# Performance work log

Hardware: AMD Instinct MI355X
Metric: run time of the kernel (lower is better)

## Reference

```python
import jax, jax.numpy as jnp
import numpy as np

NUM_EXPERTS = 16
NUM_K = 2


def setup_inputs() -> dict:
    key = jax.random.key(0)
    k1, k2 = jax.random.split(key)
    x = jax.random.normal(k1, (8, 8192, 1024), dtype=jnp.float32)
    W = jax.random.normal(k2, (NUM_EXPERTS, 1024), dtype=jnp.float32) * (1.0 / np.sqrt(1024))
    b = jnp.zeros((NUM_EXPERTS,), dtype=jnp.float32)
    return {"x": x, "W": W, "b": b}


def reference(x, W, b):
    # logits: [B, S, E]
    logits = jnp.einsum('bsd,ed->bse', x, W) + b
    weights = jax.nn.softmax(logits, axis=-1)
    # top-k over experts, then scatter values back into a sparse gate mask
    topk_vals, topk_idx = jax.lax.top_k(weights, NUM_K)  # [B, S, k]
    # one-hot scatter (E is small, so [B,S,k,E] intermediate is cheap)
    gated = (jax.nn.one_hot(topk_idx, NUM_EXPERTS, dtype=weights.dtype)
             * topk_vals[..., None]).sum(axis=-2)  # [B, S, E]
    # permute(2, 0, 1): [E, B, S]
    return gated.transpose(2, 0, 1), weights.transpose(2, 0, 1)
```

## Files before the change

### kernel.cpp

```cpp
#include <hip/hip_runtime.h>
#include <math.h>


typedef __attribute__((ext_vector_type(8))) short frag8;
typedef __attribute__((ext_vector_type(4))) float f32x4;
typedef unsigned short u16;
typedef unsigned int u32;

constexpr int D    = 1024;
constexpr int D4   = 256;
constexpr int NE   = 16;
constexpr int NTOK = 65536;
constexpr int TPB  = 256;
constexpr int TOKS = 64;
constexpr int NCH  = 16;
constexpr int RS   = 72;
constexpr int PL   = TOKS * RS;
constexpr int LSTR = 20;

__device__ __forceinline__ u16 bf_rne(float v, float* back) {
    u32 u = __float_as_uint(v);
    u32 r = (u + 0x7FFFu + ((u >> 16) & 1u)) >> 16;
    *back = __uint_as_float(r << 16);
    return (u16)r;
}

__device__ __forceinline__ void split3(float v, u16& a, u16& b, u16& c) {
    float t;
    a = bf_rne(v, &t); float r = v - t;
    b = bf_rne(r, &t); r -= t;
    c = bf_rne(r, &t);
}

__device__ __forceinline__ void loadX(const float4* __restrict__ xg4, int c,
                                      int tid, float4* pf) {
    const int col = tid & 15;
    #pragma unroll
    for (int s = 0; s < 4; ++s) {
        const int r = (s << 4) + (tid >> 4);
        pf[s] = xg4[r * D4 + c * 16 + col];
    }
}

__device__ __forceinline__ void loadB(const u16* __restrict__ wb, int c,
                                      frag8 Bf[2][3]) {
    #pragma unroll
    for (int ks = 0; ks < 2; ++ks)
        #pragma unroll
        for (int p = 0; p < 3; ++p)
            Bf[ks][p] = *(const frag8*)(wb + p * (NE * D) + (c * 2 + ks) * 32);
}

__device__ __forceinline__ void stage(const float4* pf, u16* __restrict__ lbuf,
                                      int tid) {
    const int col = tid & 15;
    #pragma unroll
    for (int s = 0; s < 4; ++s) {
        const int r = (s << 4) + (tid >> 4);
        u16 h[3][4];
        split3(pf[s].x, h[0][0], h[1][0], h[2][0]);
        split3(pf[s].y, h[0][1], h[1][1], h[2][1]);
        split3(pf[s].z, h[0][2], h[1][2], h[2][2]);
        split3(pf[s].w, h[0][3], h[1][3], h[2][3]);
        #pragma unroll
        for (int p = 0; p < 3; ++p) {
            u32 lo = (u32)h[p][0] | ((u32)h[p][1] << 16);
            u32 hi = (u32)h[p][2] | ((u32)h[p][3] << 16);
            *(uint2*)&lbuf[p * PL + r * RS + (col << 2)] = make_uint2(lo, hi);
        }
    }
}

__device__ __forceinline__ void compute(const u16* __restrict__ lbuf,
                                        const frag8 Bf[2][3],
                                        int l, int w, f32x4& acc) {
    const u16* arow = lbuf + (w * 16 + (l & 15)) * RS + (l >> 4) * 8;
    #pragma unroll
    for (int ks = 0; ks < 2; ++ks) {
        frag8 a1 = *(const frag8*)(arow + 0 * PL + ks * 32);
        frag8 a2 = *(const frag8*)(arow + 1 * PL + ks * 32);
        frag8 a3 = *(const frag8*)(arow + 2 * PL + ks * 32);
        acc = __builtin_amdgcn_mfma_f32_16x16x32_bf16(a3, Bf[ks][0], acc, 0, 0, 0);
        acc = __builtin_amdgcn_mfma_f32_16x16x32_bf16(a2, Bf[ks][1], acc, 0, 0, 0);
        acc = __builtin_amdgcn_mfma_f32_16x16x32_bf16(a1, Bf[ks][2], acc, 0, 0, 0);
        acc = __builtin_amdgcn_mfma_f32_16x16x32_bf16(a2, Bf[ks][0], acc, 0, 0, 0);
        acc = __builtin_amdgcn_mfma_f32_16x16x32_bf16(a1, Bf[ks][1], acc, 0, 0, 0);
        acc = __builtin_amdgcn_mfma_f32_16x16x32_bf16(a1, Bf[ks][0], acc, 0, 0, 0);
    }
}

__global__ void prep_w(const float* __restrict__ W, u16* __restrict__ wsp) {
    const int i = blockIdx.x * 256 + threadIdx.x;
    if (i < NE * D) {
        u16 a, b, c;
        split3(W[i], a, b, c);
        wsp[i] = a; wsp[NE * D + i] = b; wsp[2 * NE * D + i] = c;
    }
}

__global__ __launch_bounds__(TPB, 2) void gating_mfma(
    const float* __restrict__ x,
    const float* __restrict__ bias,
    const u16* __restrict__ wsp,
    float* __restrict__ out)
{
    __shared__ __align__(16) u16 xls[2 * 3 * PL];
    const int tid = threadIdx.x;
    const int l = tid & 63, w = tid >> 6;
    const long blockTok = (long)blockIdx.x * TOKS;
    const float4* __restrict__ xg4 = (const float4*)x + blockTok * D4;
    const u16* __restrict__ wb = wsp + (l & 15) * D + (l >> 4) * 8;

    float4 pfA[4], pfB[4];
    frag8 BfA[2][3], BfB[2][3];
    loadX(xg4, 0, tid, pfA);
    loadB(wb, 0, BfA);
    f32x4 acc = {0.f, 0.f, 0.f, 0.f};

    #pragma unroll 1
    for (int c = 0; c < NCH; c += 2) {
        stage(pfA, xls, tid);
        __syncthreads();
        loadX(xg4, c + 1, tid, pfB);
        loadB(wb, c + 1, BfB);
        compute(xls, BfA, l, w, acc);

        stage(pfB, xls + 3 * PL, tid);
        __syncthreads();
        if (c + 2 < NCH) { loadX(xg4, c + 2, tid, pfA); loadB(wb, c + 2, BfA); }
        compute(xls + 3 * PL, BfB, l, w, acc);
    }

    float* lb = (float*)xls;
    #pragma unroll
    for (int r = 0; r < 4; ++r)
        lb[(w * 16 + (l >> 4) * 4 + r) * LSTR + (l & 15)] = acc[r];
    __syncthreads();

    float logits[NE];
    float mx = -INFINITY;
    #pragma unroll
    for (int e = 0; e < NE; ++e) {
        logits[e] = lb[l * LSTR + e] + bias[e];
        mx = fmaxf(mx, logits[e]);
    }
    float wt[NE];
    float s = 0.0f;
    #pragma unroll
    for (int e = 0; e < NE; ++e) { wt[e] = __expf(logits[e] - mx); s += wt[e]; }
    const float inv = 1.0f / s;
    #pragma unroll
    for (int e = 0; e < NE; ++e) wt[e] *= inv;

    float b1 = -1.0f; int i1 = 0;
    float b2 = -1.0f; int i2 = 0;
    #pragma unroll
    for (int e = 0; e < NE; ++e) {
        if (wt[e] > b1)      { b2 = b1; i2 = i1; b1 = wt[e]; i1 = e; }
        else if (wt[e] > b2) { b2 = wt[e]; i2 = e; }
    }

    float* __restrict__ out0 = out;
    float* __restrict__ out1 = out + (long)NE * NTOK;
    #pragma unroll
    for (int i = 0; i < 4; ++i) {
        const int e = w * 4 + i;
        const float g = (e == i1) ? b1 : ((e == i2) ? b2 : 0.0f);
        out0[(long)e * NTOK + blockTok + l] = g;
        out1[(long)e * NTOK + blockTok + l] = wt[e];
    }
}

extern "C" void kernel_launch(void* const* d_in, const int* in_sizes, int n_in,
                              void* d_out, int out_size, void* d_ws, size_t ws_size,
                              hipStream_t stream) {
    const float* x = (const float*)d_in[0];
    const float* W = (const float*)d_in[1];
    const float* b = (const float*)d_in[2];
    float* out = (float*)d_out;
    u16* wsp = (u16*)d_ws;

    prep_w<<<64, 256, 0, stream>>>(W, wsp);
    gating_mfma<<<NTOK / TOKS, TPB, 0, stream>>>(x, b, wsp, out);
}
```

Baseline: 381.3 us.

## Stream raw fp32 x into swizzled LDS via async loads, split at MFMA time

Replaces the register-prefetch path, which split x into three bf16 planes before writing them to LDS, with direct global-to-LDS async loads of the raw fp32 tiles. The tiles are stored with an XOR column swizzle, and each lane splits its own fragment into bf16 parts just before the MFMAs. This cuts LDS footprint and VGPR pressure, so launch bounds rise to four blocks per CU, and it removes the register staging round trip. The cost is that the split arithmetic now sits on the compute side. Correctness also relies on the barrier waiting for the async LDS writes to finish.

```diff
diff --git a/kernel.cpp b/kernel.cpp
--- a/kernel.cpp
+++ b/kernel.cpp
@@ -8,14 +8,12 @@
 typedef unsigned int u32;
 
 constexpr int D    = 1024;
-constexpr int D4   = 256;
 constexpr int NE   = 16;
 constexpr int NTOK = 65536;
 constexpr int TPB  = 256;
 constexpr int TOKS = 64;
 constexpr int NCH  = 16;
-constexpr int RS   = 72;
-constexpr int PL   = TOKS * RS;
+constexpr int BUFF = 4096;
 constexpr int LSTR = 20;
 
 __device__ __forceinline__ u16 bf_rne(float v, float* back) {
@@ -32,14 +30,20 @@
     c = bf_rne(r, &t);
 }
 
-__device__ __forceinline__ void loadX(const float4* __restrict__ xg4, int c,
-                                      int tid, float4* pf) {
-    const int col = tid & 15;
-    #pragma unroll
-    for (int s = 0; s < 4; ++s) {
-        const int r = (s << 4) + (tid >> 4);
-        pf[s] = xg4[r * D4 + c * 16 + col];
-    }
+__device__ __forceinline__ void split2pk(float lo, float hi,
+                                         u32& p1, u32& p2, u32& p3) {
+    u16 a0, b0, c0, a1, b1, c1;
+    split3(lo, a0, b0, c0);
+    split3(hi, a1, b1, c1);
+    p1 = (u32)a0 | ((u32)a1 << 16);
+    p2 = (u32)b0 | ((u32)b1 << 16);
+    p3 = (u32)c0 | ((u32)c1 << 16);
+}
+
+__device__ __forceinline__ void async16(const float* g, float* l) {
+    __builtin_amdgcn_global_load_lds(
+        (const __attribute__((address_space(1))) void*)g,
+        (__attribute__((address_space(3))) void*)l, 16, 0, 0);
 }
 
 __device__ __forceinline__ void loadB(const u16* __restrict__ wb, int c,
@@ -51,41 +55,30 @@
             Bf[ks][p] = *(const frag8*)(wb + p * (NE * D) + (c * 2 + ks) * 32);
 }
 
-__device__ __forceinline__ void stage(const float4* pf, u16* __restrict__ lbuf,
-                                      int tid) {
-    const int col = tid & 15;
-    #pragma unroll
-    for (int s = 0; s < 4; ++s) {
-        const int r = (s << 4) + (tid >> 4);
-        u16 h[3][4];
-        split3(pf[s].x, h[0][0], h[1][0], h[2][0]);
-        split3(pf[s].y, h[0][1], h[1][1], h[2][1]);
-        split3(pf[s].z, h[0][2], h[1][2], h[2][2]);
-        split3(pf[s].w, h[0][3], h[1][3], h[2][3]);
-        #pragma unroll
-        for (int p = 0; p < 3; ++p) {
-            u32 lo = (u32)h[p][0] | ((u32)h[p][1] << 16);
-            u32 hi = (u32)h[p][2] | ((u32)h[p][3] << 16);
-            *(uint2*)&lbuf[p * PL + r * RS + (col << 2)] = make_uint2(lo, hi);
-        }
-    }
-}
-
-__device__ __forceinline__ void compute(const u16* __restrict__ lbuf,
-                                        const frag8 Bf[2][3],
-                                        int l, int w, f32x4& acc) {
-    const u16* arow = lbuf + (w * 16 + (l & 15)) * RS + (l >> 4) * 8;
+union Pk { u32 d[4]; frag8 f; };
+
+__device__ __forceinline__ void computeChunk(const float* __restrict__ buf,
+                                             const frag8 Bf[2][3],
+                                             int rtok, int xsw, int cbb,
+                                             f32x4& acc) {
+    const float* arow = buf + rtok * 64;
     #pragma unroll
     for (int ks = 0; ks < 2; ++ks) {
-        frag8 a1 = *(const frag8*)(arow + 0 * PL + ks * 32);
-        frag8 a2 = *(const frag8*)(arow + 1 * PL + ks * 32);
-        frag8 a3 = *(const frag8*)(arow + 2 * PL + ks * 32);
-        acc = __builtin_amdgcn_mfma_f32_16x16x32_bf16(a3, Bf[ks][0], acc, 0, 0, 0);
-        acc = __builtin_amdgcn_mfma_f32_16x16x32_bf16(a2, Bf[ks][1], acc, 0, 0, 0);
-        acc = __builtin_amdgcn_mfma_f32_16x16x32_bf16(a1, Bf[ks][2], acc, 0, 0, 0);
-        acc = __builtin_amdgcn_mfma_f32_16x16x32_bf16(a2, Bf[ks][0], acc, 0, 0, 0);
-        acc = __builtin_amdgcn_mfma_f32_16x16x32_bf16(a1, Bf[ks][1], acc, 0, 0, 0);
-        acc = __builtin_amdgcn_mfma_f32_16x16x32_bf16(a1, Bf[ks][0], acc, 0, 0, 0);
+        const int c0 = (cbb + ks * 8) ^ xsw;
+        const int c1 = (cbb + ks * 8 + 1) ^ xsw;
+        const float4 f0 = *(const float4*)(arow + c0 * 4);
+        const float4 f1 = *(const float4*)(arow + c1 * 4);
+        Pk P1, P2, P3;
+        split2pk(f0.x, f0.y, P1.d[0], P2.d[0], P3.d[0]);
+        split2pk(f0.z, f0.w, P1.d[1], P2.d[1], P3.d[1]);
+        split2pk(f1.x, f1.y, P1.d[2], P2.d[2], P3.d[2]);
+        split2pk(f1.z, f1.w, P1.d[3], P2.d[3], P3.d[3]);
+        acc = __builtin_amdgcn_mfma_f32_16x16x32_bf16(P3.f, Bf[ks][0], acc, 0, 0, 0);
+        acc = __builtin_amdgcn_mfma_f32_16x16x32_bf16(P2.f, Bf[ks][1], acc, 0, 0, 0);
+        acc = __builtin_amdgcn_mfma_f32_16x16x32_bf16(P1.f, Bf[ks][2], acc, 0, 0, 0);
+        acc = __builtin_amdgcn_mfma_f32_16x16x32_bf16(P2.f, Bf[ks][0], acc, 0, 0, 0);
+        acc = __builtin_amdgcn_mfma_f32_16x16x32_bf16(P1.f, Bf[ks][1], acc, 0, 0, 0);
+        acc = __builtin_amdgcn_mfma_f32_16x16x32_bf16(P1.f, Bf[ks][0], acc, 0, 0, 0);
     }
 }
 
@@ -98,43 +91,66 @@
     }
 }
 
-__global__ __launch_bounds__(TPB, 2) void gating_mfma(
+__global__ __launch_bounds__(TPB, 4) void gating_mfma(
     const float* __restrict__ x,
     const float* __restrict__ bias,
     const u16* __restrict__ wsp,
     float* __restrict__ out)
 {
-    __shared__ __align__(16) u16 xls[2 * 3 * PL];
+    __shared__ __align__(16) float xls[2 * BUFF];
     const int tid = threadIdx.x;
-    const int l = tid & 63, w = tid >> 6;
+    const int l   = tid & 63;
+    const int wvu = __builtin_amdgcn_readfirstlane(tid >> 6);
     const long blockTok = (long)blockIdx.x * TOKS;
-    const float4* __restrict__ xg4 = (const float4*)x + blockTok * D4;
+
+    const float* gp[4];
+    #pragma unroll
+    for (int i = 0; i < 4; ++i) {
+        const int s  = wvu * 256 + i * 64 + l;
+        const int r  = s >> 4;
+        const int cb = (s & 15) ^ (r & 15);
+        gp[i] = x + (blockTok + r) * D + cb * 4;
+    }
+
     const u16* __restrict__ wb = wsp + (l & 15) * D + (l >> 4) * 8;
-
-    float4 pfA[4], pfB[4];
+    const int rtok = wvu * 16 + (l & 15);
+    const int xsw  = l & 15;
+    const int cbb  = (l >> 4) * 2;
+
     frag8 BfA[2][3], BfB[2][3];
-    loadX(xg4, 0, tid, pfA);
+    #pragma unroll
+    for (int i = 0; i < 4; ++i)
+        async16((float*)gp[i], &xls[wvu * 1024 + i * 256]);
     loadB(wb, 0, BfA);
     f32x4 acc = {0.f, 0.f, 0.f, 0.f};
 
     #pragma unroll 1
     for (int c = 0; c < NCH; c += 2) {
-        stage(pfA, xls, tid);
         __syncthreads();
-        loadX(xg4, c + 1, tid, pfB);
-        loadB(wb, c + 1, BfB);
-        compute(xls, BfA, l, w, acc);
-
-        stage(pfB, xls + 3 * PL, tid);
+        if (true) {
+            #pragma unroll
+            for (int i = 0; i < 4; ++i)
+                async16((float*)(gp[i] + (c + 1) * 64),
+                        &xls[BUFF + wvu * 1024 + i * 256]);
+            loadB(wb, c + 1, BfB);
+        }
+        computeChunk(xls, BfA, rtok, xsw, cbb, acc);
+
         __syncthreads();
-        if (c + 2 < NCH) { loadX(xg4, c + 2, tid, pfA); loadB(wb, c + 2, BfA); }
-        compute(xls + 3 * PL, BfB, l, w, acc);
+        if (c + 2 < NCH) {
+            #pragma unroll
+            for (int i = 0; i < 4; ++i)
+                async16((float*)(gp[i] + (c + 2) * 64),
+                        &xls[wvu * 1024 + i * 256]);
+            loadB(wb, c + 2, BfA);
+        }
+        computeChunk(xls + BUFF, BfB, rtok, xsw, cbb, acc);
     }
 
     float* lb = (float*)xls;
     #pragma unroll
     for (int r = 0; r < 4; ++r)
-        lb[(w * 16 + (l >> 4) * 4 + r) * LSTR + (l & 15)] = acc[r];
+        lb[(wvu * 16 + (l >> 4) * 4 + r) * LSTR + (l & 15)] = acc[r];
     __syncthreads();
 
     float logits[NE];
@@ -164,7 +180,7 @@
     float* __restrict__ out1 = out + (long)NE * NTOK;
     #pragma unroll
     for (int i = 0; i < 4; ++i) {
-        const int e = w * 4 + i;
+        const int e = wvu * 4 + i;
         const float g = (e == i1) ? b1 : ((e == i2) ? b2 : 0.0f);
         out0[(long)e * NTOK + blockTok + l] = g;
         out1[(long)e * NTOK + blockTok + l] = wt[e];
```

Result: no change. 375.5 us (-1.5%).
